# Performance work log

Hardware: AMD Instinct MI355X
Metric: run time of the kernel (lower is better)

The kernel has to match this reference:

```python
import jax, jax.numpy as jnp
import numpy as np
from jax import lax

B, L, LQ, D_IN, ET, H, INIT_EMBED = 16, 256, 64, 32, 128, 4, 8
DIM = 2 * D_IN          # attention value/feature dim (x concat mask)
ETK = ET // H           # per-head time-embedding dim


def _lin(key, fan_in, shape):
    b = 1.0 / np.sqrt(fan_in)
    return jax.random.uniform(key, shape, jnp.float32, -b, b)


def setup_inputs() -> dict:
    key = jax.random.key(0)
    ks = jax.random.split(key, 24)
    inp = {
        "x": jax.random.normal(ks[0], (B, L, D_IN), jnp.float32),
        "time_steps": jnp.sort(jax.random.uniform(ks[1], (B, L), jnp.float32), axis=-1),
        "mask": (jax.random.uniform(ks[2], (B, L, D_IN)) > 0.5).astype(jnp.float32),
        "query": jnp.linspace(0.0, 1.0, LQ, dtype=jnp.float32),
        # time embedding: Linear(1,1) and Linear(1, ET-1)
        "w_lin": _lin(ks[3], 1, (1,)), "b_lin": _lin(ks[4], 1, (1,)),
        "w_per": _lin(ks[5], 1, (ET - 1,)), "b_per": _lin(ks[6], 1, (ET - 1,)),
        # attention projections (stored as (in,out))
        "Wq": _lin(ks[7], ET, (ET, ET)), "bq": _lin(ks[8], ET, (ET,)),
        "Wk": _lin(ks[9], ET, (ET, ET)), "bk": _lin(ks[10], ET, (ET,)),
        "Wo": _lin(ks[11], H * DIM, (H * DIM, ET)), "bo": _lin(ks[12], H * DIM, (ET,)),
        # vanilla RNN (tanh)
        "W_ih": _lin(ks[13], ET, (ET, ET)), "b_ih": _lin(ks[14], ET, (ET,)),
        "W_hh": _lin(ks[15], ET, (ET, ET)), "b_hh": _lin(ks[16], ET, (ET,)),
        "r1_w": _lin(ks[17], ET, (ET, 128)), "r1_b": _lin(ks[17], ET, (128,)),
        "r2_w": _lin(ks[18], 128, (128, 128)), "r2_b": _lin(ks[18], 128, (128,)),
        "r3_w": _lin(ks[19], 128, (128, ET)), "r3_b": _lin(ks[19], 128, (ET,)),
        "r4_w": _lin(ks[20], ET, (ET, INIT_EMBED)), "r4_b": _lin(ks[20], ET, (INIT_EMBED,)),
    }
    return inp


def reference(x, time_steps, mask, query,
              w_lin, b_lin, w_per, b_per,
              Wq, bq, Wk, bk, Wo, bo,
              W_ih, b_ih, W_hh, b_hh,
              r1_w, r1_b, r2_w, r2_b, r3_w, r3_b, r4_w, r4_b):
    def time_embed(tt):  # (...,) -> (..., ET)
        tt = tt[..., None]
        return jnp.concatenate([tt * w_lin + b_lin,
                                jnp.sin(tt * w_per + b_per)], axis=-1)

    xc = jnp.concatenate([x, mask], axis=-1)          # (B,L,DIM) value
    m2 = jnp.concatenate([mask, mask], axis=-1)       # (B,L,DIM)

    kemb = time_embed(time_steps)                     # (B,L,ET)
    qemb = time_embed(query)                          # (LQ,ET)

    q = (qemb @ Wq + bq).reshape(LQ, H, ETK).transpose(1, 0, 2)       # (H,LQ,ETK)
    k = (kemb @ Wk + bk).reshape(B, L, H, ETK).transpose(0, 2, 1, 3)  # (B,H,L,ETK)

    scores = jnp.einsum('hqe,bhke->bhqk', q, k) / np.sqrt(ETK)        # (B,H,LQ,L)
    # per-feature mask broadcast: (B,H,LQ,L,DIM)
    s5 = jnp.where(m2[:, None, None, :, :] == 0, -1e9, scores[..., None])
    p = jax.nn.softmax(s5, axis=-2)                   # softmax over keys L
    att = jnp.einsum('bhqkd,bkd->bhqd', p, xc)        # (B,H,LQ,DIM)
    att = att.transpose(0, 2, 1, 3).reshape(B, LQ, H * DIM)
    out = att @ Wo + bo                               # (B,LQ,ET)

    # vanilla tanh RNN, return final hidden state
    def step(h, xt):
        h = jnp.tanh(xt @ W_ih + b_ih + h @ W_hh + b_hh)
        return h, None
    h0 = jnp.zeros((B, ET), out.dtype)
    hT, _ = lax.scan(step, h0, out.transpose(1, 0, 2))  # scan over LQ

    y = hT @ r1_w + r1_b
    y = y @ r2_w + r2_b
    y = y @ r3_w + r3_b
    y = y @ r4_w + r4_b                               # (B, INIT_EMBED)
    return y
```

## Files before the change

### kernel.cpp

```cpp
#include <hip/hip_runtime.h>
#include <hip/hip_bf16.h>


#define NB 16
#define NL 256
#define NLQ 64
#define NDIN 32
#define NET 128
#define NH 4
#define NETK 32

#define HPAD 136
#define PAD(i) ((i) + 4 * ((i) >> 6))

__global__ __launch_bounds__(128) void k_embed_proj(
    const float* __restrict__ ts, const float* __restrict__ query,
    const float* __restrict__ w_lin, const float* __restrict__ b_lin,
    const float* __restrict__ w_per, const float* __restrict__ b_per,
    const float* __restrict__ Wk, const float* __restrict__ bk,
    const float* __restrict__ Wq, const float* __restrict__ bq,
    float* __restrict__ kproj, float* __restrict__ qproj) {
  __shared__ float emb[8 * NET];
  int g = blockIdx.x;
  int j = threadIdx.x;
  bool isQ = (g >= 512);
  int base = (isQ ? g - 512 : g) * 8;
  float wl_ = w_lin[0], bl_ = b_lin[0];
  float wp = (j > 0) ? w_per[j - 1] : 0.f;
  float bp = (j > 0) ? b_per[j - 1] : 0.f;
#pragma unroll
  for (int rr = 0; rr < 8; rr++) {
    float t = isQ ? query[base + rr] : ts[base + rr];
    emb[rr * NET + j] = (j == 0) ? (t * wl_ + bl_) : sinf(t * wp + bp);
  }
  __syncthreads();
  const float* W = isQ ? Wq : Wk;
  float bias = isQ ? bq[j] : bk[j];
  float acc[8];
#pragma unroll
  for (int rr = 0; rr < 8; rr++) acc[rr] = bias;
#pragma unroll 4
  for (int i = 0; i < NET; i++) {
    float wv = W[i * NET + j];
#pragma unroll
    for (int rr = 0; rr < 8; rr++) acc[rr] += emb[rr * NET + i] * wv;
  }
  float* dst = isQ ? qproj : kproj;
#pragma unroll
  for (int rr = 0; rr < 8; rr++) dst[(size_t)(base + rr) * NET + j] = acc[rr];
}

__global__ __launch_bounds__(256) void k_attn(
    const float* __restrict__ x, const float* __restrict__ mask,
    const float* __restrict__ qproj, const float* __restrict__ kproj,
    float* __restrict__ att) {
  const float SC = 0.17677669529663687f;
  int blk = blockIdx.x;
  int qg = blk & 15;
  int h  = (blk >> 4) & 3;
  int b  = blk >> 6;
  int t  = threadIdx.x;

  __shared__ float xs[NL * NDIN];
  __shared__ unsigned mb[NL];
  __shared__ float es[4 * NL];
  __shared__ float qs[4 * NETK];

  if (t < 128) {
    int qq = t >> 5, i = t & 31;
    qs[t] = qproj[(qg * 4 + qq) * NET + h * NETK + i];
  }
  {
    const float4* src = (const float4*)(x + (size_t)b * NL * NDIN);
    float4* dst = (float4*)xs;
#pragma unroll
    for (int u = 0; u < 8; u++) dst[t + 256 * u] = src[t + 256 * u];
  }
  {
    const float4* mr4 = (const float4*)(mask + (size_t)(b * NL + t) * NDIN);
    unsigned bits = 0;
#pragma unroll
    for (int u = 0; u < 8; u++) {
      float4 m = mr4[u];
      bits |= (m.x != 0.f ? 1u : 0u) << (4 * u);
      bits |= (m.y != 0.f ? 1u : 0u) << (4 * u + 1);
      bits |= (m.z != 0.f ? 1u : 0u) << (4 * u + 2);
      bits |= (m.w != 0.f ? 1u : 0u) << (4 * u + 3);
    }
    mb[t] = bits;
  }
  __syncthreads();

  {
    float kr[NETK];
    const float4* kp =
        (const float4*)(kproj + (size_t)(b * NL + t) * NET + h * NETK);
#pragma unroll
    for (int i = 0; i < 8; i++) {
      float4 v = kp[i];
      kr[4 * i] = v.x; kr[4 * i + 1] = v.y;
      kr[4 * i + 2] = v.z; kr[4 * i + 3] = v.w;
    }
#pragma unroll
    for (int qq = 0; qq < 4; qq++) {
      const float* qv = &qs[qq * NETK];
      float s0 = 0.f, s1 = 0.f;
#pragma unroll
      for (int i = 0; i < NETK; i += 2) {
        s0 += qv[i] * kr[i];
        s1 += qv[i + 1] * kr[i + 1];
      }
      es[qq * NL + t] = __expf((s0 + s1) * SC);
    }
  }
  __syncthreads();

  {
    int s = t & 1;
    int p = t >> 1;
    int qq = p >> 5;
    int c  = p & 31;
    int k0 = s * 128;
    float den = 0.f, num = 0.f, sumx = 0.f;
#pragma unroll 4
    for (int k = k0; k < k0 + 128; k++) {
      float e  = es[qq * NL + k];
      float mv = ((mb[k] >> c) & 1u) ? 1.f : 0.f;
      float xv = xs[k * NDIN + c];
      sumx += xv;
      e *= mv;
      den += e;
      num += e * xv;
    }
    den  += __shfl_xor(den, 1, 64);
    num  += __shfl_xor(num, 1, 64);
    sumx += __shfl_xor(sumx, 1, 64);
    if (s == 0) {
      bool any = (den > 0.f);
      float ax = any ? (num / den) : (sumx * (1.f / 256.f));
      float am = any ? 1.f : 0.f;
      int q = qg * 4 + qq;
      float* ao = att + (size_t)((b * NLQ + q) * NH + h) * 64;
      ao[c]      = ax;
      ao[32 + c] = am;
    }
  }
}

__global__ __launch_bounds__(128) void k_out_xw(
    const float* __restrict__ att,
    const float* __restrict__ Wo, const float* __restrict__ bo,
    const float* __restrict__ Wih, const float* __restrict__ bih,
    const float* __restrict__ bhh, float* __restrict__ XW) {
  int r = blockIdx.x;
  int j = threadIdx.x;
  __shared__ float arow[NH * 64];
  __shared__ float orow[NET];
  arow[j]       = att[(size_t)r * 256 + j];
  arow[j + 128] = att[(size_t)r * 256 + 128 + j];
  __syncthreads();
  float a0 = bo[j], a1 = 0.f, a2 = 0.f, a3 = 0.f;
#pragma unroll 8
  for (int u = 0; u < 256; u += 4) {
    a0 += arow[u]     * Wo[(u)     * NET + j];
    a1 += arow[u + 1] * Wo[(u + 1) * NET + j];
    a2 += arow[u + 2] * Wo[(u + 2) * NET + j];
    a3 += arow[u + 3] * Wo[(u + 3) * NET + j];
  }
  orow[j] = (a0 + a1) + (a2 + a3);
  __syncthreads();
  float b0 = bih[j] + bhh[j], b1 = 0.f, b2 = 0.f, b3 = 0.f;
#pragma unroll 8
  for (int e = 0; e < NET; e += 4) {
    b0 += orow[e]     * Wih[(e)     * NET + j];
    b1 += orow[e + 1] * Wih[(e + 1) * NET + j];
    b2 += orow[e + 2] * Wih[(e + 2) * NET + j];
    b3 += orow[e + 3] * Wih[(e + 3) * NET + j];
  }
  XW[(size_t)r * NET + j] = (b0 + b1) + (b2 + b3);
}

__device__ __forceinline__ void layer128(const float* src_lds,
                                         const float* __restrict__ W,
                                         const float* __restrict__ bvec,
                                         float* dst_lds, int j, int s) {
  const float4* h4 = (const float4*)(src_lds + s * 68);
  float a0 = 0.f, a1 = 0.f, a2 = 0.f, a3 = 0.f;
#pragma unroll
  for (int i = 0; i < 16; i++) {
    float4 hv = h4[i];
    int base = (s * 64 + 4 * i) * NET + j;
    a0 += hv.x * W[base];
    a1 += hv.y * W[base + NET];
    a2 += hv.z * W[base + 2 * NET];
    a3 += hv.w * W[base + 3 * NET];
  }
  float acc = (a0 + a1) + (a2 + a3);
  acc += __shfl_xor(acc, 1, 64);
  if (s == 0) dst_lds[PAD(j)] = acc + bvec[j];
}

__global__ __launch_bounds__(256, 1) void k_rnn(
    const float* __restrict__ XW, const float* __restrict__ Whh,
    const float* __restrict__ r1w, const float* __restrict__ r1b,
    const float* __restrict__ r2w, const float* __restrict__ r2b,
    const float* __restrict__ r3w, const float* __restrict__ r3b,
    const float* __restrict__ r4w, const float* __restrict__ r4b,
    float* __restrict__ out) {
  int b = blockIdx.x;
  int tid = threadIdx.x;
  int s = tid & 1;
  int j = tid >> 1;
  __shared__ float xwl[NLQ * NET];
  __shared__ float hb[2][HPAD];
  __shared__ float tmp[HPAD];

  {
    const float4* src = (const float4*)(XW + (size_t)b * NLQ * NET);
    float4* dst = (float4*)xwl;
#pragma unroll
    for (int u = 0; u < 8; u++) dst[tid + 256 * u] = src[tid + 256 * u];
  }
  float w[64];
#pragma unroll
  for (int i = 0; i < 64; i++) w[i] = Whh[(s * 64 + i) * NET + j];

  if (tid < 128) hb[0][PAD(tid)] = 0.f;
  __syncthreads();

  for (int t = 0; t < NLQ; t++) {
    float xwv = xwl[t * NET + j];
    const float4* h4 = (const float4*)&hb[t & 1][s * 68];
    float a0 = 0.f, a1 = 0.f, a2 = 0.f, a3 = 0.f;
#pragma unroll
    for (int i = 0; i < 16; i++) {
      float4 hv = h4[i];
      a0 += hv.x * w[4 * i];
      a1 += hv.y * w[4 * i + 1];
      a2 += hv.z * w[4 * i + 2];
      a3 += hv.w * w[4 * i + 3];
    }
    float acc = (a0 + a1) + (a2 + a3);
    acc += __shfl_xor(acc, 1, 64);
    if (s == 0) {
      float z = acc + xwv;
      float e2 = __expf(2.f * z);
      hb[(t + 1) & 1][PAD(j)] = 1.f - 2.f / (e2 + 1.f);
    }
    __syncthreads();
  }

  layer128(hb[0], r1w, r1b, tmp, j, s);
  __syncthreads();
  layer128(tmp, r2w, r2b, hb[1], j, s);
  __syncthreads();
  layer128(hb[1], r3w, r3b, hb[0], j, s);
  __syncthreads();
  if (tid < 64) {
    int jj = tid >> 3, p = tid & 7;
    float y = 0.f;
#pragma unroll
    for (int i = 0; i < 16; i++) {
      int ii = p * 16 + i;
      y += hb[0][PAD(ii)] * r4w[ii * 8 + jj];
    }
    y += __shfl_xor(y, 1, 64);
    y += __shfl_xor(y, 2, 64);
    y += __shfl_xor(y, 4, 64);
    if (p == 0) out[b * 8 + jj] = y + r4b[jj];
  }
}

extern "C" void kernel_launch(void* const* d_in, const int* in_sizes, int n_in,
                              void* d_out, int out_size, void* d_ws, size_t ws_size,
                              hipStream_t stream) {
  const float* x     = (const float*)d_in[0];
  const float* ts    = (const float*)d_in[1];
  const float* mask  = (const float*)d_in[2];
  const float* query = (const float*)d_in[3];
  const float* w_lin = (const float*)d_in[4];
  const float* b_lin = (const float*)d_in[5];
  const float* w_per = (const float*)d_in[6];
  const float* b_per = (const float*)d_in[7];
  const float* Wq    = (const float*)d_in[8];
  const float* bq    = (const float*)d_in[9];
  const float* Wk    = (const float*)d_in[10];
  const float* bk    = (const float*)d_in[11];
  const float* Wo    = (const float*)d_in[12];
  const float* bo    = (const float*)d_in[13];
  const float* Wih   = (const float*)d_in[14];
  const float* bih   = (const float*)d_in[15];
  const float* Whh   = (const float*)d_in[16];
  const float* bhh   = (const float*)d_in[17];
  const float* r1w   = (const float*)d_in[18];
  const float* r1b   = (const float*)d_in[19];
  const float* r2w   = (const float*)d_in[20];
  const float* r2b   = (const float*)d_in[21];
  const float* r3w   = (const float*)d_in[22];
  const float* r3b   = (const float*)d_in[23];
  const float* r4w   = (const float*)d_in[24];
  const float* r4b   = (const float*)d_in[25];
  float* out = (float*)d_out;

  float* ws    = (float*)d_ws;
  float* kproj = ws;
  float* qproj = ws + 524288;
  float* att   = ws + 532480;
  float* XW    = ws + 794624;

  k_embed_proj<<<520, 128, 0, stream>>>(
      ts, query, w_lin, b_lin, w_per, b_per, Wk, bk, Wq, bq, kproj, qproj);
  k_attn<<<NB * NH * 16, 256, 0, stream>>>(x, mask, qproj, kproj, att);
  k_out_xw<<<NB * NLQ, 128, 0, stream>>>(att, Wo, bo, Wih, bih, bhh, XW);
  k_rnn<<<NB, 256, 0, stream>>>(XW, Whh, r1w, r1b, r2w, r2b, r3w, r3b,
                                r4w, r4b, out);
}
```

Before: 184.6 us.

## Run RNN recurrence in a single wavefront using readlane broadcasts

The sequential tanh RNN kernel now runs as one 64-lane wavefront per batch instead of 256 threads. Each lane holds two hidden units and 256 Whh weights in registers, and broadcasts the hidden state with readlane instead of going through LDS. This removes the per-timestep __syncthreads and LDS round-trips on the serial critical path. The cost is a lot more serial FMA work per lane (256 per step instead of 64) and very high register pressure, which risks spills. The regressor layers are reworked the same way.

```diff
diff --git a/kernel.cpp b/kernel.cpp
--- a/kernel.cpp
+++ b/kernel.cpp
@@ -9,9 +9,6 @@
 #define NET 128
 #define NH 4
 #define NETK 32
-
-#define HPAD 136
-#define PAD(i) ((i) + 4 * ((i) >> 6))
 
 __global__ __launch_bounds__(128) void k_embed_proj(
     const float* __restrict__ ts, const float* __restrict__ query,
@@ -180,27 +177,32 @@
   XW[(size_t)r * NET + j] = (b0 + b1) + (b2 + b3);
 }
 
-__device__ __forceinline__ void layer128(const float* src_lds,
+__device__ __forceinline__ float bcast(float v, int i) {
+  return __int_as_float(__builtin_amdgcn_readlane(__float_as_int(v), i));
+}
+
+__device__ __forceinline__ void layer_rl(float& slo, float& shi,
                                          const float* __restrict__ W,
                                          const float* __restrict__ bvec,
-                                         float* dst_lds, int j, int s) {
-  const float4* h4 = (const float4*)(src_lds + s * 68);
-  float a0 = 0.f, a1 = 0.f, a2 = 0.f, a3 = 0.f;
-#pragma unroll
-  for (int i = 0; i < 16; i++) {
-    float4 hv = h4[i];
-    int base = (s * 64 + 4 * i) * NET + j;
-    a0 += hv.x * W[base];
-    a1 += hv.y * W[base + NET];
-    a2 += hv.z * W[base + 2 * NET];
-    a3 += hv.w * W[base + 3 * NET];
-  }
-  float acc = (a0 + a1) + (a2 + a3);
-  acc += __shfl_xor(acc, 1, 64);
-  if (s == 0) dst_lds[PAD(j)] = acc + bvec[j];
-}
-
-__global__ __launch_bounds__(256, 1) void k_rnn(
+                                         int l) {
+  float a = bvec[l], c = bvec[64 + l];
+  float slo_in = slo, shi_in = shi;
+#pragma unroll
+  for (int i = 0; i < 64; i++) {
+    float s = bcast(slo_in, i);
+    a += s * W[i * NET + l];
+    c += s * W[i * NET + 64 + l];
+  }
+#pragma unroll
+  for (int i = 0; i < 64; i++) {
+    float s = bcast(shi_in, i);
+    a += s * W[(64 + i) * NET + l];
+    c += s * W[(64 + i) * NET + 64 + l];
+  }
+  slo = a; shi = c;
+}
+
+__global__ __launch_bounds__(64, 1) void k_rnn(
     const float* __restrict__ XW, const float* __restrict__ Whh,
     const float* __restrict__ r1w, const float* __restrict__ r1b,
     const float* __restrict__ r2w, const float* __restrict__ r2b,
@@ -208,66 +210,66 @@
     const float* __restrict__ r4w, const float* __restrict__ r4b,
     float* __restrict__ out) {
   int b = blockIdx.x;
-  int tid = threadIdx.x;
-  int s = tid & 1;
-  int j = tid >> 1;
+  int l = threadIdx.x;
   __shared__ float xwl[NLQ * NET];
-  __shared__ float hb[2][HPAD];
-  __shared__ float tmp[HPAD];
 
   {
     const float4* src = (const float4*)(XW + (size_t)b * NLQ * NET);
     float4* dst = (float4*)xwl;
 #pragma unroll
-    for (int u = 0; u < 8; u++) dst[tid + 256 * u] = src[tid + 256 * u];
-  }
-  float w[64];
-#pragma unroll
-  for (int i = 0; i < 64; i++) w[i] = Whh[(s * 64 + i) * NET + j];
-
-  if (tid < 128) hb[0][PAD(tid)] = 0.f;
+    for (int u = 0; u < 32; u++) dst[l + 64 * u] = src[l + 64 * u];
+  }
+
+  float w00[64], w01[64], w10[64], w11[64];
+#pragma unroll
+  for (int i = 0; i < 64; i++) w00[i] = Whh[i * NET + l];
+#pragma unroll
+  for (int i = 0; i < 64; i++) w01[i] = Whh[(64 + i) * NET + l];
+#pragma unroll
+  for (int i = 0; i < 64; i++) w10[i] = Whh[i * NET + l + 64];
+#pragma unroll
+  for (int i = 0; i < 64; i++) w11[i] = Whh[(64 + i) * NET + l + 64];
+
+  float hlo = 0.f, hhi = 0.f;
   __syncthreads();
 
   for (int t = 0; t < NLQ; t++) {
-    float xwv = xwl[t * NET + j];
-    const float4* h4 = (const float4*)&hb[t & 1][s * 68];
-    float a0 = 0.f, a1 = 0.f, a2 = 0.f, a3 = 0.f;
-#pragma unroll
-    for (int i = 0; i < 16; i++) {
-      float4 hv = h4[i];
-      a0 += hv.x * w[4 * i];
-      a1 += hv.y * w[4 * i + 1];
-      a2 += hv.z * w[4 * i + 2];
-      a3 += hv.w * w[4 * i + 3];
-    }
-    float acc = (a0 + a1) + (a2 + a3);
-    acc += __shfl_xor(acc, 1, 64);
-    if (s == 0) {
-      float z = acc + xwv;
-      float e2 = __expf(2.f * z);
-      hb[(t + 1) & 1][PAD(j)] = 1.f - 2.f / (e2 + 1.f);
-    }
-    __syncthreads();
-  }
-
-  layer128(hb[0], r1w, r1b, tmp, j, s);
-  __syncthreads();
-  layer128(tmp, r2w, r2b, hb[1], j, s);
-  __syncthreads();
-  layer128(hb[1], r3w, r3b, hb[0], j, s);
-  __syncthreads();
-  if (tid < 64) {
-    int jj = tid >> 3, p = tid & 7;
+    float xw0 = xwl[t * NET + l];
+    float xw1 = xwl[t * NET + 64 + l];
+    float hl = hlo, hh = hhi;
+    float a0 = 0.f, a1 = 0.f, c0 = 0.f, c1 = 0.f;
+#pragma unroll
+    for (int i = 0; i < 64; i++) {
+      float s = bcast(hl, i);
+      a0 += s * w00[i];
+      c0 += s * w10[i];
+    }
+#pragma unroll
+    for (int i = 0; i < 64; i++) {
+      float s = bcast(hh, i);
+      a1 += s * w01[i];
+      c1 += s * w11[i];
+    }
+    float z0 = (a0 + a1) + xw0;
+    float z1 = (c0 + c1) + xw1;
+    float e0 = __expf(2.f * z0);
+    float e1 = __expf(2.f * z1);
+    hlo = 1.f - 2.f / (e0 + 1.f);
+    hhi = 1.f - 2.f / (e1 + 1.f);
+  }
+
+  layer_rl(hlo, hhi, r1w, r1b, l);
+  layer_rl(hlo, hhi, r2w, r2b, l);
+  layer_rl(hlo, hhi, r3w, r3b, l);
+  {
+    int jj = l & 7;
     float y = 0.f;
-#pragma unroll
-    for (int i = 0; i < 16; i++) {
-      int ii = p * 16 + i;
-      y += hb[0][PAD(ii)] * r4w[ii * 8 + jj];
-    }
-    y += __shfl_xor(y, 1, 64);
-    y += __shfl_xor(y, 2, 64);
-    y += __shfl_xor(y, 4, 64);
-    if (p == 0) out[b * 8 + jj] = y + r4b[jj];
+    float slo_in = hlo, shi_in = hhi;
+#pragma unroll
+    for (int i = 0; i < 64; i++) y += bcast(slo_in, i) * r4w[i * 8 + jj];
+#pragma unroll
+    for (int i = 0; i < 64; i++) y += bcast(shi_in, i) * r4w[(64 + i) * 8 + jj];
+    if (l < 8) out[b * 8 + l] = y + r4b[l];
   }
 }
 
@@ -312,6 +314,6 @@
       ts, query, w_lin, b_lin, w_per, b_per, Wk, bk, Wq, bq, kproj, qproj);
   k_attn<<<NB * NH * 16, 256, 0, stream>>>(x, mask, qproj, kproj, att);
   k_out_xw<<<NB * NLQ, 128, 0, stream>>>(att, Wo, bo, Wih, bih, bhh, XW);
-  k_rnn<<<NB, 256, 0, stream>>>(XW, Whh, r1w, r1b, r2w, r2b, r3w, r3b,
-                                r4w, r4b, out);
-}
+  k_rnn<<<NB, 64, 0, stream>>>(XW, Whh, r1w, r1b, r2w, r2b, r3w, r3b,
+                               r4w, r4b, out);
+}
```

Result: slower. 238.0 us (+28.9%).
